# Kernel tuning notes

Measured on AMD Instinct MI355X. Metric: run time of the kernel, lower is better.

## Reference

```python
import jax, jax.numpy as jnp
import numpy as np


def setup_inputs() -> dict:
    N, E, F_IN, H, C = 100000, 3200000, 128, 16, 2
    key = jax.random.key(0)
    k1, k2, k3, k4 = jax.random.split(key, 4)
    x = jax.random.normal(k1, (N, F_IN), dtype=jnp.float32)
    edge_index = jax.random.randint(k2, (2, E), 0, N, dtype=jnp.int64)
    W1 = jax.random.normal(k3, (F_IN, H), dtype=jnp.float32) * (1.0 / np.sqrt(F_IN))
    b1 = jnp.zeros((H,), dtype=jnp.float32)
    W2 = jax.random.normal(k4, (H, C), dtype=jnp.float32) * (1.0 / np.sqrt(H))
    b2 = jnp.zeros((C,), dtype=jnp.float32)
    return {"x": x, "edge_index": edge_index, "W1": W1, "b1": b1, "W2": W2, "b2": b2}


def _gcn_norm(edge_index, num_nodes):
    # PyG gcn_norm: add self-loops, deg from destination, norm = d^-1/2[src]*d^-1/2[dst]
    loop = jnp.arange(num_nodes, dtype=edge_index.dtype)
    src = jnp.concatenate([edge_index[0], loop])
    dst = jnp.concatenate([edge_index[1], loop])
    deg = jax.ops.segment_sum(jnp.ones_like(src, dtype=jnp.float32), dst,
                              num_segments=num_nodes)
    dinv = jnp.where(deg > 0, jax.lax.rsqrt(deg), 0.0)
    norm = dinv[src] * dinv[dst]  # [E + N]
    return src, dst, norm


def _gcn_conv(h, src, dst, norm, W, b, num_nodes):
    h = h @ W                       # dense transform first (in >= out channels)
    msg = h[src] * norm[:, None]    # gather + normalize, [E+N, out]
    agg = jax.ops.segment_sum(msg, dst, num_segments=num_nodes)
    return agg + b


def reference(x, edge_index, W1, b1, W2, b2):
    N = x.shape[0]
    src, dst, norm = _gcn_norm(edge_index, N)
    h = jax.nn.relu(_gcn_conv(x, src, dst, norm, W1, b1, N))
    out = _gcn_conv(h, src, dst, norm, W2, b2, N)
    return out
```

## Files before the change

### kernel.cpp

```cpp
#include <hip/hip_runtime.h>


#define EPB 8192
#define CAP 16384

typedef unsigned int u32;
typedef unsigned short u16;

__device__ __forceinline__ float bflo(u32 u) { return __uint_as_float(u << 16); }
__device__ __forceinline__ float bfhi(u32 u) { return __uint_as_float(u & 0xffff0000u); }
__device__ __forceinline__ u32 pack_bf2(float a, float b) {
    u32 ua = __float_as_uint(a); ua = (ua + 0x7fffu + ((ua >> 16) & 1u)) >> 16;
    u32 ub = __float_as_uint(b); ub = (ub + 0x7fffu + ((ub >> 16) & 1u)) >> 16;
    return ua | (ub << 16);
}

__global__ __launch_bounds__(512) void k_bzero(int* __restrict__ gcnt, int NBUK) {
    int t = threadIdx.x;
    if (t < NBUK) gcnt[t] = 0;
}

__global__ __launch_bounds__(512) void k_count(const int* __restrict__ dst,
                                               int* __restrict__ gcnt,
                                               u16* __restrict__ bhist,
                                               int E, int NBUK) {
    __shared__ int hist[512];
    int tid = threadIdx.x;
    hist[tid] = 0;
    __syncthreads();
    int base = blockIdx.x * EPB;
    int end = base + EPB; if (end > E) end = E;
    for (int e = base + tid; e < end; e += 512)
        atomicAdd(&hist[dst[e] >> 8], 1);
    __syncthreads();
    int v = hist[tid];
    if (tid < NBUK) {
        if (v) atomicAdd(&gcnt[tid], v);
        bhist[(size_t)blockIdx.x * 512 + tid] = (u16)v;
    }
}

__global__ __launch_bounds__(512) void k_bscan(const int* __restrict__ gcnt,
                                               int* __restrict__ gbase,
                                               int* __restrict__ gcur,
                                               int* __restrict__ rp,
                                               int N, int E, int NBUK) {
    __shared__ int s[512];
    int tid = threadIdx.x;
    int v = (tid < NBUK) ? gcnt[tid] : 0;
    s[tid] = v;
    __syncthreads();
    for (int o = 1; o < 512; o <<= 1) {
        int t = (tid >= o) ? s[tid - o] : 0;
        __syncthreads();
        s[tid] += t;
        __syncthreads();
    }
    if (tid < NBUK) { int b = s[tid] - v; gbase[tid] = b; gcur[tid] = b; }
    if (tid == 0) rp[N] = E;
}

__global__ __launch_bounds__(512) void k_scatter(const int* __restrict__ ei,
                                                 const u16* __restrict__ bhist,
                                                 int* __restrict__ gcur,
                                                 u32* __restrict__ part,
                                                 int E, int NBUK) {
    __shared__ int hist[512];
    __shared__ int lofs[512];
    __shared__ int rbase[512];
    __shared__ u32 buf[EPB];
    int tid = threadIdx.x;
    int v = (tid < NBUK) ? (int)bhist[(size_t)blockIdx.x * 512 + tid] : 0;
    lofs[tid] = v;
    __syncthreads();
    for (int o = 1; o < 512; o <<= 1) {
        int t = (tid >= o) ? lofs[tid - o] : 0;
        __syncthreads();
        lofs[tid] += t;
        __syncthreads();
    }
    int excl = lofs[tid] - v;
    int rb = 0;
    if (tid < NBUK && v > 0) rb = atomicAdd(&gcur[tid], v);
    rbase[tid] = rb - excl;
    hist[tid] = excl;
    lofs[tid] = excl;
    __syncthreads();
    int base = blockIdx.x * EPB;
    int end = base + EPB; if (end > E) end = E;
    for (int e = base + tid; e < end; e += 512) {
        int s = ei[e], d = ei[E + e];
        int pos = atomicAdd(&hist[d >> 8], 1);
        buf[pos] = ((u32)(d & 255) << 24) | (u32)s;
    }
    __syncthreads();
    int cnt = end - base;
    for (int j = tid; j < cnt; j += 512) {
        int lo = 0, hi = NBUK - 1;
        while (lo < hi) {
            int mid = (lo + hi + 1) >> 1;
            if (lofs[mid] <= j) lo = mid; else hi = mid - 1;
        }
        part[rbase[lo] + j] = buf[j];
    }
}

__global__ __launch_bounds__(512) void k_fillB(u32* __restrict__ part,
                                               const int* __restrict__ gbase,
                                               const int* __restrict__ gcnt,
                                               int* __restrict__ rp,
                                               float* __restrict__ dinv, int N) {
    __shared__ int hist[256];
    __shared__ int ofs[256];
    __shared__ u32 srcbuf[CAP];
    int b = blockIdx.x, tid = threadIdx.x;
    int base = gbase[b], cnt = gcnt[b];
    if (tid < 256) hist[tid] = 0;
    __syncthreads();
    for (int j = tid; j < cnt; j += 512)
        atomicAdd(&hist[part[base + j] >> 24], 1);
    __syncthreads();
    int v = 0;
    if (tid < 256) { v = hist[tid]; ofs[tid] = v; }
    __syncthreads();
    for (int o = 1; o < 256; o <<= 1) {
        int t = 0;
        if (tid < 256 && tid >= o) t = ofs[tid - o];
        __syncthreads();
        if (tid < 256) ofs[tid] += t;
        __syncthreads();
    }
    int excl = 0;
    if (tid < 256) { excl = ofs[tid] - v; hist[tid] = excl; }
    __syncthreads();
    for (int j = tid; j < cnt; j += 512) {
        u32 pv = part[base + j];
        int pos = atomicAdd(&hist[pv >> 24], 1);
        if (pos < CAP) srcbuf[pos] = pv & 0xFFFFFFu;
    }
    __syncthreads();
    for (int j = tid; j < cnt; j += 512)
        part[base + j] = srcbuf[j];
    int d = b * 256 + tid;
    if (tid < 256 && d < N) {
        rp[d] = base + excl;
        dinv[d] = rsqrtf((float)(v + 1));
    }
}

__global__ __launch_bounds__(256) void k_xw1(const float* __restrict__ x,
                                             const float* __restrict__ W1,
                                             const float* __restrict__ dinv,
                                             u16* __restrict__ hs, int N) {
    __shared__ float w[4 * 516];
    int tid = threadIdx.x;
    for (int t = tid; t < 2048; t += 256)
        w[(t >> 9) * 516 + (t & 511)] = W1[t];
    __syncthreads();
    int t = blockIdx.x * 256 + tid;
    int n = t >> 2, q = t & 3;
    if (n >= N) return;
    const float4* xr = (const float4*)(x + (size_t)n * 128 + q * 32);
    const float* ws = w + q * 516;
    float acc[16];
    #pragma unroll
    for (int c = 0; c < 16; ++c) acc[c] = 0.f;
    #pragma unroll
    for (int i = 0; i < 8; ++i) {
        float4 u = xr[i];
        const float4* wf = (const float4*)(ws + i * 64);
        #pragma unroll
        for (int c4 = 0; c4 < 4; ++c4) {
            float4 wa = wf[c4];
            float4 wb = wf[4 + c4];
            float4 wc = wf[8 + c4];
            float4 wd = wf[12 + c4];
            int c = c4 * 4;
            acc[c+0] = fmaf(u.x, wa.x, acc[c+0]); acc[c+1] = fmaf(u.x, wa.y, acc[c+1]);
            acc[c+2] = fmaf(u.x, wa.z, acc[c+2]); acc[c+3] = fmaf(u.x, wa.w, acc[c+3]);
            acc[c+0] = fmaf(u.y, wb.x, acc[c+0]); acc[c+1] = fmaf(u.y, wb.y, acc[c+1]);
            acc[c+2] = fmaf(u.y, wb.z, acc[c+2]); acc[c+3] = fmaf(u.y, wb.w, acc[c+3]);
            acc[c+0] = fmaf(u.z, wc.x, acc[c+0]); acc[c+1] = fmaf(u.z, wc.y, acc[c+1]);
            acc[c+2] = fmaf(u.z, wc.z, acc[c+2]); acc[c+3] = fmaf(u.z, wc.w, acc[c+3]);
            acc[c+0] = fmaf(u.w, wd.x, acc[c+0]); acc[c+1] = fmaf(u.w, wd.y, acc[c+1]);
            acc[c+2] = fmaf(u.w, wd.z, acc[c+2]); acc[c+3] = fmaf(u.w, wd.w, acc[c+3]);
        }
    }
    #pragma unroll
    for (int c = 0; c < 16; ++c) {
        acc[c] += __shfl_xor(acc[c], 1);
        acc[c] += __shfl_xor(acc[c], 2);
    }
    float di = dinv[n];
    uint2 o;
    o.x = pack_bf2(acc[4*q+0] * di, acc[4*q+1] * di);
    o.y = pack_bf2(acc[4*q+2] * di, acc[4*q+3] * di);
    ((uint2*)(hs + (size_t)n * 16))[q] = o;
}

__global__ __launch_bounds__(256) void k_agg1h2(const int* __restrict__ rp,
                                                const int* __restrict__ csr,
                                                const u16* __restrict__ hs,
                                                const float* __restrict__ dinv,
                                                const float* __restrict__ W2,
                                                const float* __restrict__ b1,
                                                float* __restrict__ h2s, int N) {
    int lane = threadIdx.x & 63;
    int wid = blockIdx.x * 16 + (threadIdx.x >> 6) * 4 + (lane >> 4);
    if (wid >= N) return;
    int l = lane & 15;
    int c4 = l & 3, g = l >> 2;
    int beg = rp[wid], end = rp[wid + 1];
    float ax = 0.f, ay = 0.f, az = 0.f, aw = 0.f;
    for (int j = beg + g; j < end; j += 4) {
        int s = csr[j];
        uint2 u = ((const uint2*)(hs + (size_t)s * 16))[c4];
        ax += bflo(u.x); ay += bfhi(u.x);
        az += bflo(u.y); aw += bfhi(u.y);
    }
    ax += __shfl_xor(ax, 4); ay += __shfl_xor(ay, 4);
    az += __shfl_xor(az, 4); aw += __shfl_xor(aw, 4);
    ax += __shfl_xor(ax, 8); ay += __shfl_xor(ay, 8);
    az += __shfl_xor(az, 8); aw += __shfl_xor(aw, 8);
    uint2 su = ((const uint2*)(hs + (size_t)wid * 16))[c4];
    ax += bflo(su.x); ay += bfhi(su.x);
    az += bflo(su.y); aw += bfhi(su.y);
    float di = dinv[wid];
    float4 bq = ((const float4*)b1)[c4];
    float vx = fmaxf(fmaf(di, ax, bq.x), 0.f);
    float vy = fmaxf(fmaf(di, ay, bq.y), 0.f);
    float vz = fmaxf(fmaf(di, az, bq.z), 0.f);
    float vw = fmaxf(fmaf(di, aw, bq.w), 0.f);
    float4 pa = ((const float4*)W2)[2 * c4];
    float4 pb = ((const float4*)W2)[2 * c4 + 1];
    float p0 = vx * pa.x + vy * pa.z + vz * pb.x + vw * pb.z;
    float p1 = vx * pa.y + vy * pa.w + vz * pb.y + vw * pb.w;
    p0 += __shfl_xor(p0, 1); p1 += __shfl_xor(p1, 1);
    p0 += __shfl_xor(p0, 2); p1 += __shfl_xor(p1, 2);
    if (l == 0)
        *(float2*)(h2s + (size_t)wid * 2) = make_float2(p0 * di, p1 * di);
}

__global__ __launch_bounds__(256) void k_agg2(const int* __restrict__ rp,
                                              const int* __restrict__ csr,
                                              const float* __restrict__ h2s,
                                              const float* __restrict__ dinv,
                                              const float* __restrict__ b2,
                                              float* __restrict__ out, int N) {
    int lane = threadIdx.x & 63;
    int wid = blockIdx.x * 16 + (threadIdx.x >> 6) * 4 + (lane >> 4);
    if (wid >= N) return;
    int l = lane & 15;
    int beg = rp[wid], end = rp[wid + 1];
    float a0 = 0.f, a1 = 0.f;
    for (int j = beg + l; j < end; j += 16) {
        int s = csr[j];
        float2 v = *(const float2*)(h2s + (size_t)s * 2);
        a0 += v.x; a1 += v.y;
    }
    a0 += __shfl_xor(a0, 1); a1 += __shfl_xor(a1, 1);
    a0 += __shfl_xor(a0, 2); a1 += __shfl_xor(a1, 2);
    a0 += __shfl_xor(a0, 4); a1 += __shfl_xor(a1, 4);
    a0 += __shfl_xor(a0, 8); a1 += __shfl_xor(a1, 8);
    if (l == 0) {
        float di = dinv[wid];
        float2 sv = *(const float2*)(h2s + (size_t)wid * 2);
        *(float2*)(out + (size_t)wid * 2) =
            make_float2(fmaf(di, a0 + sv.x, b2[0]), fmaf(di, a1 + sv.y, b2[1]));
    }
}

extern "C" void kernel_launch(void* const* d_in, const int* in_sizes, int n_in,
                              void* d_out, int out_size, void* d_ws, size_t ws_size,
                              hipStream_t stream) {
    const float* x  = (const float*)d_in[0];
    const int*   ei = (const int*)d_in[1];
    const float* W1 = (const float*)d_in[2];
    const float* b1 = (const float*)d_in[3];
    const float* W2 = (const float*)d_in[4];
    const float* b2 = (const float*)d_in[5];
    float* out = (float*)d_out;

    const int N = in_sizes[0] / 128;
    const int E = in_sizes[1] / 2;
    const int NBUK = (N + 255) / 256;
    const int NPB  = (E + EPB - 1) / EPB;

    char* ws = (char*)d_ws;
    size_t off = 0;
    auto alloc = [&](size_t bytes) {
        void* p = ws + off;
        off = (off + bytes + 255) & ~(size_t)255;
        return p;
    };
    u32*   part  = (u32*)alloc((size_t)E * 4);
    int*   rp    = (int*)alloc((size_t)(N + 1) * 4);
    float* dinv  = (float*)alloc((size_t)N * 4);
    u16*   hs    = (u16*)alloc((size_t)N * 16 * 2);
    float* h2s   = (float*)alloc((size_t)N * 2 * 4);
    int*   gcnt  = (int*)alloc((size_t)NBUK * 4);
    int*   gbase = (int*)alloc((size_t)NBUK * 4);
    int*   gcur  = (int*)alloc((size_t)NBUK * 4);
    u16*   bhist = (u16*)alloc((size_t)NPB * 512 * 2);

    k_bzero  <<<dim3(1),    dim3(512), 0, stream>>>(gcnt, NBUK);
    k_count  <<<dim3(NPB),  dim3(512), 0, stream>>>(ei + E, gcnt, bhist, E, NBUK);
    k_bscan  <<<dim3(1),    dim3(512), 0, stream>>>(gcnt, gbase, gcur, rp, N, E, NBUK);
    k_scatter<<<dim3(NPB),  dim3(512), 0, stream>>>(ei, bhist, gcur, part, E, NBUK);
    k_fillB  <<<dim3(NBUK), dim3(512), 0, stream>>>(part, gbase, gcnt, rp, dinv, N);
    k_xw1    <<<dim3((N * 4 + 255) / 256), dim3(256), 0, stream>>>(x, W1, dinv, hs, N);
    k_agg1h2 <<<dim3((N + 15) / 16), dim3(256), 0, stream>>>(rp, (const int*)part, hs, dinv, W2, b1, h2s, N);
    k_agg2   <<<dim3((N + 15) / 16), dim3(256), 0, stream>>>(rp, (const int*)part, h2s, dinv, b2, out, N);
}
```

Before: 216.2 us.

## Vectorize edge loads, store bucket ids in scatter, widen agg1 gathers

The count and scatter kernels now read edge indices as int4, and the scatter kernel records each slot's bucket id in shared memory. That replaces the per-element binary search over local offsets with a direct lookup. The layer-1 aggregation has each lane load 16 bytes (8 bf16 features) instead of 8, so 8 edges are processed in parallel per node instead of 4. The int4 loads assume 16-byte alignment of base and E offsets, and the extra shared array and doubled accumulators add register and LDS pressure.

```diff
diff --git a/kernel.cpp b/kernel.cpp
--- a/kernel.cpp
+++ b/kernel.cpp
@@ -30,7 +30,17 @@
     __syncthreads();
     int base = blockIdx.x * EPB;
     int end = base + EPB; if (end > E) end = E;
-    for (int e = base + tid; e < end; e += 512)
+    int cnt = end - base;
+    int nv = cnt >> 2;
+    const int4* d4p = (const int4*)(dst + base);
+    for (int t = tid; t < nv; t += 512) {
+        int4 d4 = d4p[t];
+        atomicAdd(&hist[d4.x >> 8], 1);
+        atomicAdd(&hist[d4.y >> 8], 1);
+        atomicAdd(&hist[d4.z >> 8], 1);
+        atomicAdd(&hist[d4.w >> 8], 1);
+    }
+    for (int e = base + (nv << 2) + tid; e < end; e += 512)
         atomicAdd(&hist[dst[e] >> 8], 1);
     __syncthreads();
     int v = hist[tid];
@@ -66,43 +76,54 @@
                                                  u32* __restrict__ part,
                                                  int E, int NBUK) {
     __shared__ int hist[512];
-    __shared__ int lofs[512];
     __shared__ int rbase[512];
     __shared__ u32 buf[EPB];
+    __shared__ u16 bkt[EPB];
     int tid = threadIdx.x;
     int v = (tid < NBUK) ? (int)bhist[(size_t)blockIdx.x * 512 + tid] : 0;
-    lofs[tid] = v;
+    hist[tid] = v;
     __syncthreads();
     for (int o = 1; o < 512; o <<= 1) {
-        int t = (tid >= o) ? lofs[tid - o] : 0;
-        __syncthreads();
-        lofs[tid] += t;
-        __syncthreads();
-    }
-    int excl = lofs[tid] - v;
+        int t = (tid >= o) ? hist[tid - o] : 0;
+        __syncthreads();
+        hist[tid] += t;
+        __syncthreads();
+    }
+    int excl = hist[tid] - v;
     int rb = 0;
     if (tid < NBUK && v > 0) rb = atomicAdd(&gcur[tid], v);
     rbase[tid] = rb - excl;
     hist[tid] = excl;
-    lofs[tid] = excl;
     __syncthreads();
     int base = blockIdx.x * EPB;
     int end = base + EPB; if (end > E) end = E;
-    for (int e = base + tid; e < end; e += 512) {
+    int cnt = end - base;
+    int nv = cnt >> 2;
+    const int4* s4p = (const int4*)(ei + base);
+    const int4* d4p = (const int4*)(ei + E + base);
+    for (int t = tid; t < nv; t += 512) {
+        int4 s4 = s4p[t];
+        int4 d4 = d4p[t];
+        int b, pos;
+        b = d4.x >> 8; pos = atomicAdd(&hist[b], 1);
+        buf[pos] = ((u32)(d4.x & 255) << 24) | (u32)s4.x; bkt[pos] = (u16)b;
+        b = d4.y >> 8; pos = atomicAdd(&hist[b], 1);
+        buf[pos] = ((u32)(d4.y & 255) << 24) | (u32)s4.y; bkt[pos] = (u16)b;
+        b = d4.z >> 8; pos = atomicAdd(&hist[b], 1);
+        buf[pos] = ((u32)(d4.z & 255) << 24) | (u32)s4.z; bkt[pos] = (u16)b;
+        b = d4.w >> 8; pos = atomicAdd(&hist[b], 1);
+        buf[pos] = ((u32)(d4.w & 255) << 24) | (u32)s4.w; bkt[pos] = (u16)b;
+    }
+    for (int e = base + (nv << 2) + tid; e < end; e += 512) {
         int s = ei[e], d = ei[E + e];
-        int pos = atomicAdd(&hist[d >> 8], 1);
+        int b = d >> 8;
+        int pos = atomicAdd(&hist[b], 1);
         buf[pos] = ((u32)(d & 255) << 24) | (u32)s;
-    }
-    __syncthreads();
-    int cnt = end - base;
-    for (int j = tid; j < cnt; j += 512) {
-        int lo = 0, hi = NBUK - 1;
-        while (lo < hi) {
-            int mid = (lo + hi + 1) >> 1;
-            if (lofs[mid] <= j) lo = mid; else hi = mid - 1;
-        }
-        part[rbase[lo] + j] = buf[j];
-    }
+        bkt[pos] = (u16)b;
+    }
+    __syncthreads();
+    for (int j = tid; j < cnt; j += 512)
+        part[rbase[bkt[j]] + j] = buf[j];
 }
 
 __global__ __launch_bounds__(512) void k_fillB(u32* __restrict__ part,
@@ -209,34 +230,53 @@
     int wid = blockIdx.x * 16 + (threadIdx.x >> 6) * 4 + (lane >> 4);
     if (wid >= N) return;
     int l = lane & 15;
-    int c4 = l & 3, g = l >> 2;
+    int half = l & 1, g = l >> 1;
     int beg = rp[wid], end = rp[wid + 1];
-    float ax = 0.f, ay = 0.f, az = 0.f, aw = 0.f;
-    for (int j = beg + g; j < end; j += 4) {
+    float a0 = 0.f, a1 = 0.f, a2 = 0.f, a3 = 0.f;
+    float a4 = 0.f, a5 = 0.f, a6 = 0.f, a7 = 0.f;
+    for (int j = beg + g; j < end; j += 8) {
         int s = csr[j];
-        uint2 u = ((const uint2*)(hs + (size_t)s * 16))[c4];
-        ax += bflo(u.x); ay += bfhi(u.x);
-        az += bflo(u.y); aw += bfhi(u.y);
-    }
-    ax += __shfl_xor(ax, 4); ay += __shfl_xor(ay, 4);
-    az += __shfl_xor(az, 4); aw += __shfl_xor(aw, 4);
-    ax += __shfl_xor(ax, 8); ay += __shfl_xor(ay, 8);
-    az += __shfl_xor(az, 8); aw += __shfl_xor(aw, 8);
-    uint2 su = ((const uint2*)(hs + (size_t)wid * 16))[c4];
-    ax += bflo(su.x); ay += bfhi(su.x);
-    az += bflo(su.y); aw += bfhi(su.y);
+        uint4 u = ((const uint4*)(hs + (size_t)s * 16))[half];
+        a0 += bflo(u.x); a1 += bfhi(u.x);
+        a2 += bflo(u.y); a3 += bfhi(u.y);
+        a4 += bflo(u.z); a5 += bfhi(u.z);
+        a6 += bflo(u.w); a7 += bfhi(u.w);
+    }
+    a0 += __shfl_xor(a0, 2); a1 += __shfl_xor(a1, 2);
+    a2 += __shfl_xor(a2, 2); a3 += __shfl_xor(a3, 2);
+    a4 += __shfl_xor(a4, 2); a5 += __shfl_xor(a5, 2);
+    a6 += __shfl_xor(a6, 2); a7 += __shfl_xor(a7, 2);
+    a0 += __shfl_xor(a0, 4); a1 += __shfl_xor(a1, 4);
+    a2 += __shfl_xor(a2, 4); a3 += __shfl_xor(a3, 4);
+    a4 += __shfl_xor(a4, 4); a5 += __shfl_xor(a5, 4);
+    a6 += __shfl_xor(a6, 4); a7 += __shfl_xor(a7, 4);
+    a0 += __shfl_xor(a0, 8); a1 += __shfl_xor(a1, 8);
+    a2 += __shfl_xor(a2, 8); a3 += __shfl_xor(a3, 8);
+    a4 += __shfl_xor(a4, 8); a5 += __shfl_xor(a5, 8);
+    a6 += __shfl_xor(a6, 8); a7 += __shfl_xor(a7, 8);
+    uint4 su = ((const uint4*)(hs + (size_t)wid * 16))[half];
+    a0 += bflo(su.x); a1 += bfhi(su.x);
+    a2 += bflo(su.y); a3 += bfhi(su.y);
+    a4 += bflo(su.z); a5 += bfhi(su.z);
+    a6 += bflo(su.w); a7 += bfhi(su.w);
     float di = dinv[wid];
-    float4 bq = ((const float4*)b1)[c4];
-    float vx = fmaxf(fmaf(di, ax, bq.x), 0.f);
-    float vy = fmaxf(fmaf(di, ay, bq.y), 0.f);
-    float vz = fmaxf(fmaf(di, az, bq.z), 0.f);
-    float vw = fmaxf(fmaf(di, aw, bq.w), 0.f);
-    float4 pa = ((const float4*)W2)[2 * c4];
-    float4 pb = ((const float4*)W2)[2 * c4 + 1];
-    float p0 = vx * pa.x + vy * pa.z + vz * pb.x + vw * pb.z;
-    float p1 = vx * pa.y + vy * pa.w + vz * pb.y + vw * pb.w;
+    float4 bA = ((const float4*)b1)[half * 2];
+    float4 bB = ((const float4*)b1)[half * 2 + 1];
+    float v0 = fmaxf(fmaf(di, a0, bA.x), 0.f);
+    float v1 = fmaxf(fmaf(di, a1, bA.y), 0.f);
+    float v2 = fmaxf(fmaf(di, a2, bA.z), 0.f);
+    float v3 = fmaxf(fmaf(di, a3, bA.w), 0.f);
+    float v4 = fmaxf(fmaf(di, a4, bB.x), 0.f);
+    float v5 = fmaxf(fmaf(di, a5, bB.y), 0.f);
+    float v6 = fmaxf(fmaf(di, a6, bB.z), 0.f);
+    float v7 = fmaxf(fmaf(di, a7, bB.w), 0.f);
+    const float4* w4 = (const float4*)W2 + half * 4;
+    float4 q0 = w4[0], q1 = w4[1], q2 = w4[2], q3 = w4[3];
+    float p0 = v0*q0.x + v1*q0.z + v2*q1.x + v3*q1.z
+             + v4*q2.x + v5*q2.z + v6*q3.x + v7*q3.z;
+    float p1 = v0*q0.y + v1*q0.w + v2*q1.y + v3*q1.w
+             + v4*q2.y + v5*q2.w + v6*q3.y + v7*q3.w;
     p0 += __shfl_xor(p0, 1); p1 += __shfl_xor(p1, 1);
-    p0 += __shfl_xor(p0, 2); p1 += __shfl_xor(p1, 2);
     if (l == 0)
         *(float2*)(h2s + (size_t)wid * 2) = make_float2(p0 * di, p1 * di);
 }
```

After: 201.4 us. 6.9% less time.
